# Kernel optimization log

Measured on AMD Instinct MI355X. Metric: run time of the kernel, lower is better.

Reference implementation:

```python
import jax, jax.numpy as jnp
import numpy as np

E, N, D = 800000, 50000, 64

def setup_inputs() -> dict:
    key = jax.random.key(0)
    k0, k1, k2, k3 = jax.random.split(key, 4)
    return {
        "edge_attrs": jax.random.normal(k0, (E, D), dtype=jnp.float32),
        "proj_W": jax.random.normal(k1, (D, D), dtype=jnp.float32) / np.float32(np.sqrt(D)),
        "proj_b": jnp.zeros((D,), dtype=jnp.float32),
        "upd_W": jax.random.normal(k2, (D, D), dtype=jnp.float32) / np.float32(np.sqrt(D)),
        "upd_b": jnp.zeros((D,), dtype=jnp.float32),
        "dst": jax.random.randint(k3, (E,), 0, N, dtype=jnp.int32),
        "n_nodes": N,
    }

def reference(edge_attrs, proj_W, proj_b, upd_W, upd_b, dst, n_nodes):
    # Project each edge attribute: node_projectors[e.type](e.data)
    proj = edge_attrs @ proj_W + proj_b                      # [E, D]
    # Mean-aggregate incoming edges per destination node (MeanAggregator)
    summed = jax.ops.segment_sum(proj, dst, num_segments=n_nodes)          # [N, D]
    counts = jax.ops.segment_sum(jnp.ones((dst.shape[0], 1), proj.dtype),
                                 dst, num_segments=n_nodes)                # [N, 1]
    aggregated = summed / jnp.maximum(counts, 1.0)           # nodes w/o edges -> 0
    # Per-node update: updaters(aggregated)
    return aggregated @ upd_W + upd_b                        # [N, D]
```

## Files before the change

### kernel.cpp

```cpp
#include <hip/hip_runtime.h>
#include <hip/hip_bf16.h>

#define D 64

typedef float f32x4 __attribute__((ext_vector_type(4)));
typedef float f32x2 __attribute__((ext_vector_type(2)));

__global__ void zero_kernel(int4* __restrict__ p, int n4) {
    int i = blockIdx.x * blockDim.x + threadIdx.x;
    if (i < n4) p[i] = make_int4(0, 0, 0, 0);
}

__global__ void count_kernel(const int4* __restrict__ dst4, int* __restrict__ counts, int E4) {
    int i = blockIdx.x * blockDim.x + threadIdx.x;
    if (i < E4) {
        int4 d = dst4[i];
        atomicAdd(&counts[d.x], 1);
        atomicAdd(&counts[d.y], 1);
        atomicAdd(&counts[d.z], 1);
        atomicAdd(&counts[d.w], 1);
    }
}

__global__ void blocksum_kernel(const int* __restrict__ counts, int* __restrict__ bsums, int N) {
    int t = threadIdx.x;
    int i = blockIdx.x * 256 + t;
    int v = (i < N) ? counts[i] : 0;
    int lane = t & 63, wave = t >> 6;
    #pragma unroll
    for (int o = 1; o < 64; o <<= 1) v += __shfl_xor(v, o);
    __shared__ int ws[4];
    if (lane == 0) ws[wave] = v;
    __syncthreads();
    if (t == 0) bsums[blockIdx.x] = ws[0] + ws[1] + ws[2] + ws[3];
}

__global__ void blockscan_kernel(const int* __restrict__ bsums, int* __restrict__ boffs,
                                 int* __restrict__ offsets, int N, int nb,
                                 const float* __restrict__ Wp, const float* __restrict__ Wu,
                                 const float* __restrict__ bp,
                                 float* __restrict__ Wc, float* __restrict__ bc) {
    __shared__ int wsum[16];
    __shared__ float wu[D * D];
    __shared__ float wp[D * D];
    int t = threadIdx.x;
    for (int i = t; i < D * D; i += 1024) { wu[i] = Wu[i]; wp[i] = Wp[i]; }

    int wave = t >> 6, lane = t & 63;
    int v = (t < nb) ? bsums[t] : 0;
    int s = v;
    #pragma unroll
    for (int off = 1; off < 64; off <<= 1) {
        int x = __shfl_up(s, off);
        if (lane >= off) s += x;
    }
    if (lane == 63) wsum[wave] = s;
    __syncthreads();
    int wbase = 0, total = 0;
    #pragma unroll
    for (int w = 0; w < 16; ++w) {
        int x = wsum[w];
        total += x;
        if (w < wave) wbase += x;
    }
    if (t < nb) boffs[t] = s - v + wbase;
    if (t == 0) offsets[N] = total;

    for (int idx = t; idx < D * D; idx += 1024) {
        int d = idx >> 6, j = idx & 63;
        float acc = 0.f;
        #pragma unroll
        for (int k = 0; k < D; ++k) acc = fmaf(wp[d * D + k], wu[k * D + j], acc);
        Wc[idx] = acc;
    }
    if (t < D) {
        float acc = 0.f;
        #pragma unroll
        for (int k = 0; k < D; ++k) acc = fmaf(bp[k], wu[k * D + t], acc);
        bc[t] = acc;
    }
}

__global__ void scatter_scan_kernel(const int* __restrict__ counts, const int* __restrict__ boffs,
                                    int* __restrict__ offsets, int* __restrict__ cursor, int N) {
    int t = threadIdx.x;
    int i = blockIdx.x * 256 + t;
    int v = (i < N) ? counts[i] : 0;
    int lane = t & 63, wave = t >> 6;
    int s = v;
    #pragma unroll
    for (int off = 1; off < 64; off <<= 1) {
        int x = __shfl_up(s, off);
        if (lane >= off) s += x;
    }
    __shared__ int ws[4];
    if (lane == 63) ws[wave] = s;
    __syncthreads();
    int wbase = 0;
    #pragma unroll
    for (int w = 0; w < 4; ++w) if (w < wave) wbase += ws[w];
    int excl = s - v + wbase + boffs[blockIdx.x];
    if (i < N) { offsets[i] = excl; cursor[i] = excl; }
}

__global__ __launch_bounds__(256) void scatter_bf16_kernel(
        const f32x2* __restrict__ attrs2, const int* __restrict__ dst,
        int* __restrict__ cursor, ushort2* __restrict__ ebuf, int E) {
    int lane = threadIdx.x & 63;
    int stride = gridDim.x * 256;
    int E32 = E * 32;
    for (int t = blockIdx.x * 256 + threadIdx.x; t < E32; t += stride) {
        int e = t >> 5, j = t & 31;
        f32x2 v = __builtin_nontemporal_load(&attrs2[t]);
        int pos = 0;
        if ((lane & 31) == 0) pos = atomicAdd(&cursor[dst[e]], 1);
        pos = __shfl(pos, lane & 32);
        unsigned ux = __float_as_uint(v.x);
        unsigned uy = __float_as_uint(v.y);
        ux = (ux + 0x7fffu + ((ux >> 16) & 1u)) >> 16;
        uy = (uy + 0x7fffu + ((uy >> 16) & 1u)) >> 16;
        ebuf[(size_t)pos * 32 + j] = make_ushort2((unsigned short)ux, (unsigned short)uy);
    }
}

__global__ __launch_bounds__(256) void node_kernel(
        const f32x4* __restrict__ ebuf4,
        const int* __restrict__ offsets,
        const float* __restrict__ Wc, const float* __restrict__ bc,
        const float* __restrict__ ub, float* __restrict__ out, int N) {
    __shared__ float wlds[D * D];
    __shared__ float blds[D];
    __shared__ float ulds[D];
    __shared__ int soff[5];
    int t = threadIdx.x;
    int nbase = blockIdx.x * 4;
    if (t < 5) {
        int nn = nbase + t;
        soff[t] = offsets[(nn <= N) ? nn : N];
    }
    #pragma unroll
    for (int i = t; i < D * D; i += 256) wlds[i] = Wc[i];
    if (t < D) { blds[t] = bc[t]; ulds[t] = ub[t]; }
    __syncthreads();

    int wave = t >> 6, lane = t & 63;
    int n = nbase + wave;
    if (n >= N) return;

    int off = soff[wave];
    int off2 = soff[wave + 1];
    int cnt = off2 - off;

    int rsel = lane >> 3;
    int csel = lane & 7;

    float a0 = 0.f, a1 = 0.f, a2 = 0.f, a3 = 0.f, a4 = 0.f, a5 = 0.f, a6 = 0.f, a7 = 0.f;
    for (int r0 = off; r0 < off2; r0 += 8) {
        int row = r0 + rsel;
        bool valid = row < off2;
        int idx = (valid ? row : off) * 8 + csel;
        f32x4 c = ebuf4[idx];
        if (valid) {
            unsigned u0 = __float_as_uint(c.x), u1 = __float_as_uint(c.y);
            unsigned u2 = __float_as_uint(c.z), u3 = __float_as_uint(c.w);
            a0 += __uint_as_float(u0 << 16); a1 += __uint_as_float(u0 & 0xffff0000u);
            a2 += __uint_as_float(u1 << 16); a3 += __uint_as_float(u1 & 0xffff0000u);
            a4 += __uint_as_float(u2 << 16); a5 += __uint_as_float(u2 & 0xffff0000u);
            a6 += __uint_as_float(u3 << 16); a7 += __uint_as_float(u3 & 0xffff0000u);
        }
    }
    #pragma unroll
    for (int mask = 8; mask < 64; mask <<= 1) {
        a0 += __shfl_xor(a0, mask); a1 += __shfl_xor(a1, mask);
        a2 += __shfl_xor(a2, mask); a3 += __shfl_xor(a3, mask);
        a4 += __shfl_xor(a4, mask); a5 += __shfl_xor(a5, mask);
        a6 += __shfl_xor(a6, mask); a7 += __shfl_xor(a7, mask);
    }
    float inv = (cnt > 0) ? 1.f / (float)cnt : 0.f;
    float marr[8] = { a0 * inv, a1 * inv, a2 * inv, a3 * inv,
                      a4 * inv, a5 * inv, a6 * inv, a7 * inv };

    float accO = ulds[lane] + ((cnt > 0) ? blds[lane] : 0.f);
    #pragma unroll
    for (int d = 0; d < D; ++d) {
        float mv = __shfl(marr[d & 7], d >> 3);
        accO = fmaf(mv, wlds[d * D + lane], accO);
    }
    out[(size_t)n * D + lane] = accO;
}

extern "C" void kernel_launch(void* const* d_in, const int* in_sizes, int n_in,
                              void* d_out, int out_size, void* d_ws, size_t ws_size,
                              hipStream_t stream) {
    const float* edge_attrs = (const float*)d_in[0];
    const float* proj_W     = (const float*)d_in[1];
    const float* proj_b     = (const float*)d_in[2];
    const float* upd_W      = (const float*)d_in[3];
    const float* upd_b      = (const float*)d_in[4];
    const int*   dst        = (const int*)d_in[5];

    const int E = in_sizes[0] / D;
    const int N = out_size / D;
    const int nb = (N + 255) / 256;
    const int E4 = E / 4;
    const int N4 = N / 4;

    int*   counts  = (int*)d_ws;
    int*   offsets = counts + N;
    int*   cursor  = offsets + N + 1;
    int*   bsums   = cursor + N;
    int*   boffs   = bsums + nb;
    float* Wc      = (float*)(boffs + nb);
    float* bc      = Wc + D * D;
    size_t ebuf_off = (((size_t)(bc + D) - (size_t)d_ws) + 255) & ~(size_t)255;
    ushort2* ebuf   = (ushort2*)((char*)d_ws + ebuf_off);

    zero_kernel<<<(N4 + 255) / 256, 256, 0, stream>>>((int4*)counts, N4);
    count_kernel<<<(E4 + 255) / 256, 256, 0, stream>>>((const int4*)dst, counts, E4);
    blocksum_kernel<<<nb, 256, 0, stream>>>(counts, bsums, N);
    blockscan_kernel<<<1, 1024, 0, stream>>>(bsums, boffs, offsets, N, nb,
                                             proj_W, upd_W, proj_b, Wc, bc);
    scatter_scan_kernel<<<nb, 256, 0, stream>>>(counts, boffs, offsets, cursor, N);
    scatter_bf16_kernel<<<2048, 256, 0, stream>>>((const f32x2*)edge_attrs, dst,
                                                  cursor, ebuf, E);

    int blocks_n = (N + 3) / 4;
    node_kernel<<<blocks_n, 256, 0, stream>>>((const f32x4*)ebuf, offsets,
                                              Wc, bc, upd_b, (float*)d_out, N);
}
```

Measured before the change: 195.9 us.

## Convert edges in place and gather via CSR index list instead of scattering rows

Edge attributes are now converted to bf16 in their original order, and the per-node counts are taken in the same streaming pass, replacing the scatter of whole rows into node-sorted positions. A separate fill kernel builds a CSR list of edge indices per node, and the node kernel becomes grid-strided and gathers rows through that list. This removes the atomic-serialised scattered 128-byte row writes. In exchange, the node kernel does random row gathers plus an extra index read and an extra kernel launch.

```diff
diff --git a/kernel.cpp b/kernel.cpp
--- a/kernel.cpp
+++ b/kernel.cpp
@@ -11,14 +11,19 @@
     if (i < n4) p[i] = make_int4(0, 0, 0, 0);
 }
 
-__global__ void count_kernel(const int4* __restrict__ dst4, int* __restrict__ counts, int E4) {
-    int i = blockIdx.x * blockDim.x + threadIdx.x;
-    if (i < E4) {
-        int4 d = dst4[i];
-        atomicAdd(&counts[d.x], 1);
-        atomicAdd(&counts[d.y], 1);
-        atomicAdd(&counts[d.z], 1);
-        atomicAdd(&counts[d.w], 1);
+__global__ __launch_bounds__(256) void convert_count_kernel(
+        const f32x2* __restrict__ attrs2, const int* __restrict__ dst,
+        ushort2* __restrict__ ebuf, int* __restrict__ counts, int E32) {
+    int stride = gridDim.x * 256;
+    for (int c = blockIdx.x * 256 + threadIdx.x; c < E32; c += stride) {
+        f32x2 v = __builtin_nontemporal_load(&attrs2[c]);
+        unsigned ux = __float_as_uint(v.x);
+        unsigned uy = __float_as_uint(v.y);
+        ux = (ux + 0x7fffu + ((ux >> 16) & 1u)) >> 16;
+        uy = (uy + 0x7fffu + ((uy >> 16) & 1u)) >> 16;
+        ushort2 pk = make_ushort2((unsigned short)ux, (unsigned short)uy);
+        __builtin_nontemporal_store(*(unsigned*)&pk, (unsigned*)&ebuf[c]);
+        if ((c & 31) == 0) atomicAdd(&counts[dst[c >> 5]], 1);
     }
 }
 
@@ -103,90 +108,81 @@
     if (i < N) { offsets[i] = excl; cursor[i] = excl; }
 }
 
-__global__ __launch_bounds__(256) void scatter_bf16_kernel(
-        const f32x2* __restrict__ attrs2, const int* __restrict__ dst,
-        int* __restrict__ cursor, ushort2* __restrict__ ebuf, int E) {
-    int lane = threadIdx.x & 63;
-    int stride = gridDim.x * 256;
-    int E32 = E * 32;
-    for (int t = blockIdx.x * 256 + threadIdx.x; t < E32; t += stride) {
-        int e = t >> 5, j = t & 31;
-        f32x2 v = __builtin_nontemporal_load(&attrs2[t]);
-        int pos = 0;
-        if ((lane & 31) == 0) pos = atomicAdd(&cursor[dst[e]], 1);
-        pos = __shfl(pos, lane & 32);
-        unsigned ux = __float_as_uint(v.x);
-        unsigned uy = __float_as_uint(v.y);
-        ux = (ux + 0x7fffu + ((ux >> 16) & 1u)) >> 16;
-        uy = (uy + 0x7fffu + ((uy >> 16) & 1u)) >> 16;
-        ebuf[(size_t)pos * 32 + j] = make_ushort2((unsigned short)ux, (unsigned short)uy);
+__global__ void fill_kernel(const int4* __restrict__ dst4, int* __restrict__ cursor,
+                            int* __restrict__ csr, int E4) {
+    int i = blockIdx.x * blockDim.x + threadIdx.x;
+    if (i < E4) {
+        int4 d = dst4[i];
+        int e = i * 4;
+        csr[atomicAdd(&cursor[d.x], 1)] = e + 0;
+        csr[atomicAdd(&cursor[d.y], 1)] = e + 1;
+        csr[atomicAdd(&cursor[d.z], 1)] = e + 2;
+        csr[atomicAdd(&cursor[d.w], 1)] = e + 3;
     }
 }
 
 __global__ __launch_bounds__(256) void node_kernel(
         const f32x4* __restrict__ ebuf4,
-        const int* __restrict__ offsets,
+        const int* __restrict__ csr, const int* __restrict__ offsets,
         const float* __restrict__ Wc, const float* __restrict__ bc,
         const float* __restrict__ ub, float* __restrict__ out, int N) {
     __shared__ float wlds[D * D];
     __shared__ float blds[D];
     __shared__ float ulds[D];
-    __shared__ int soff[5];
-    int t = threadIdx.x;
-    int nbase = blockIdx.x * 4;
-    if (t < 5) {
-        int nn = nbase + t;
-        soff[t] = offsets[(nn <= N) ? nn : N];
-    }
+    int t = threadIdx.x;
     #pragma unroll
     for (int i = t; i < D * D; i += 256) wlds[i] = Wc[i];
     if (t < D) { blds[t] = bc[t]; ulds[t] = ub[t]; }
     __syncthreads();
 
     int wave = t >> 6, lane = t & 63;
-    int n = nbase + wave;
-    if (n >= N) return;
-
-    int off = soff[wave];
-    int off2 = soff[wave + 1];
-    int cnt = off2 - off;
-
     int rsel = lane >> 3;
     int csel = lane & 7;
-
-    float a0 = 0.f, a1 = 0.f, a2 = 0.f, a3 = 0.f, a4 = 0.f, a5 = 0.f, a6 = 0.f, a7 = 0.f;
-    for (int r0 = off; r0 < off2; r0 += 8) {
-        int row = r0 + rsel;
-        bool valid = row < off2;
-        int idx = (valid ? row : off) * 8 + csel;
-        f32x4 c = ebuf4[idx];
-        if (valid) {
-            unsigned u0 = __float_as_uint(c.x), u1 = __float_as_uint(c.y);
-            unsigned u2 = __float_as_uint(c.z), u3 = __float_as_uint(c.w);
-            a0 += __uint_as_float(u0 << 16); a1 += __uint_as_float(u0 & 0xffff0000u);
-            a2 += __uint_as_float(u1 << 16); a3 += __uint_as_float(u1 & 0xffff0000u);
-            a4 += __uint_as_float(u2 << 16); a5 += __uint_as_float(u2 & 0xffff0000u);
-            a6 += __uint_as_float(u3 << 16); a7 += __uint_as_float(u3 & 0xffff0000u);
+    int nwaves = gridDim.x * 4;
+
+    for (int n = blockIdx.x * 4 + wave; n < N; n += nwaves) {
+        int off = offsets[n];
+        int cnt = offsets[n + 1] - off;
+
+        float a0 = 0.f, a1 = 0.f, a2 = 0.f, a3 = 0.f,
+              a4 = 0.f, a5 = 0.f, a6 = 0.f, a7 = 0.f;
+        for (int base = 0; base < cnt; base += 64) {
+            int m = cnt - base; if (m > 64) m = 64;
+            int idxv = (lane < m) ? csr[off + base + lane] : 0;
+            for (int js = 0; js < m; js += 8) {
+                int s = js + rsel;
+                int e = __shfl(idxv, s);
+                bool valid = s < m;
+                f32x4 c = ebuf4[(size_t)(valid ? e : 0) * 8 + csel];
+                if (valid) {
+                    unsigned u0 = __float_as_uint(c.x), u1 = __float_as_uint(c.y);
+                    unsigned u2 = __float_as_uint(c.z), u3 = __float_as_uint(c.w);
+                    a0 += __uint_as_float(u0 << 16); a1 += __uint_as_float(u0 & 0xffff0000u);
+                    a2 += __uint_as_float(u1 << 16); a3 += __uint_as_float(u1 & 0xffff0000u);
+                    a4 += __uint_as_float(u2 << 16); a5 += __uint_as_float(u2 & 0xffff0000u);
+                    a6 += __uint_as_float(u3 << 16); a7 += __uint_as_float(u3 & 0xffff0000u);
+                }
+            }
         }
-    }
-    #pragma unroll
-    for (int mask = 8; mask < 64; mask <<= 1) {
-        a0 += __shfl_xor(a0, mask); a1 += __shfl_xor(a1, mask);
-        a2 += __shfl_xor(a2, mask); a3 += __shfl_xor(a3, mask);
-        a4 += __shfl_xor(a4, mask); a5 += __shfl_xor(a5, mask);
-        a6 += __shfl_xor(a6, mask); a7 += __shfl_xor(a7, mask);
-    }
-    float inv = (cnt > 0) ? 1.f / (float)cnt : 0.f;
-    float marr[8] = { a0 * inv, a1 * inv, a2 * inv, a3 * inv,
-                      a4 * inv, a5 * inv, a6 * inv, a7 * inv };
-
-    float accO = ulds[lane] + ((cnt > 0) ? blds[lane] : 0.f);
-    #pragma unroll
-    for (int d = 0; d < D; ++d) {
-        float mv = __shfl(marr[d & 7], d >> 3);
-        accO = fmaf(mv, wlds[d * D + lane], accO);
-    }
-    out[(size_t)n * D + lane] = accO;
+        #pragma unroll
+        for (int mask = 8; mask < 64; mask <<= 1) {
+            a0 += __shfl_xor(a0, mask); a1 += __shfl_xor(a1, mask);
+            a2 += __shfl_xor(a2, mask); a3 += __shfl_xor(a3, mask);
+            a4 += __shfl_xor(a4, mask); a5 += __shfl_xor(a5, mask);
+            a6 += __shfl_xor(a6, mask); a7 += __shfl_xor(a7, mask);
+        }
+        float inv = (cnt > 0) ? 1.f / (float)cnt : 0.f;
+        float marr[8] = { a0 * inv, a1 * inv, a2 * inv, a3 * inv,
+                          a4 * inv, a5 * inv, a6 * inv, a7 * inv };
+
+        float accO = ulds[lane] + ((cnt > 0) ? blds[lane] : 0.f);
+        #pragma unroll
+        for (int d = 0; d < D; ++d) {
+            float mv = __shfl(marr[d & 7], d >> 3);
+            accO = fmaf(mv, wlds[d * D + lane], accO);
+        }
+        out[(size_t)n * D + lane] = accO;
+    }
 }
 
 extern "C" void kernel_launch(void* const* d_in, const int* in_sizes, int n_in,
@@ -204,27 +200,28 @@
     const int nb = (N + 255) / 256;
     const int E4 = E / 4;
     const int N4 = N / 4;
+    const int E32 = E * 32;
 
     int*   counts  = (int*)d_ws;
     int*   offsets = counts + N;
     int*   cursor  = offsets + N + 1;
     int*   bsums   = cursor + N;
     int*   boffs   = bsums + nb;
-    float* Wc      = (float*)(boffs + nb);
+    int*   csr     = boffs + nb;
+    float* Wc      = (float*)(csr + E);
     float* bc      = Wc + D * D;
     size_t ebuf_off = (((size_t)(bc + D) - (size_t)d_ws) + 255) & ~(size_t)255;
     ushort2* ebuf   = (ushort2*)((char*)d_ws + ebuf_off);
 
     zero_kernel<<<(N4 + 255) / 256, 256, 0, stream>>>((int4*)counts, N4);
-    count_kernel<<<(E4 + 255) / 256, 256, 0, stream>>>((const int4*)dst, counts, E4);
+    convert_count_kernel<<<4096, 256, 0, stream>>>((const f32x2*)edge_attrs, dst,
+                                                   ebuf, counts, E32);
     blocksum_kernel<<<nb, 256, 0, stream>>>(counts, bsums, N);
     blockscan_kernel<<<1, 1024, 0, stream>>>(bsums, boffs, offsets, N, nb,
                                              proj_W, upd_W, proj_b, Wc, bc);
     scatter_scan_kernel<<<nb, 256, 0, stream>>>(counts, boffs, offsets, cursor, N);
-    scatter_bf16_kernel<<<2048, 256, 0, stream>>>((const f32x2*)edge_attrs, dst,
-                                                  cursor, ebuf, E);
-
-    int blocks_n = (N + 3) / 4;
-    node_kernel<<<blocks_n, 256, 0, stream>>>((const f32x4*)ebuf, offsets,
-                                              Wc, bc, upd_b, (float*)d_out, N);
-}
+    fill_kernel<<<(E4 + 255) / 256, 256, 0, stream>>>((const int4*)dst, cursor, csr, E4);
+
+    node_kernel<<<2048, 256, 0, stream>>>((const f32x4*)ebuf, csr, offsets,
+                                          Wc, bc, upd_b, (float*)d_out, N);
+}
```

New measurement: 210.9 us. +7.7%, slower.

## Replace per-node CSR sort with 64-node bins and LDS atomic reduction

Applied to the files above, without the earlier changes.

Edges are now counting-sorted into bins of 64 destination nodes instead of exact per-node CSR order, which removes one scan kernel and reduces cursor atomic contention. Each bin is reduced by one block that accumulates into shared memory with LDS float atomics, then applies the fused projection-update matrix. The change adds a per-edge node-id buffer and LDS atomic traffic. Float summation order becomes nondeterministic. The binscan kernel still runs in a single 1024-thread block, so it relies on nbins (782) being at most 1024.

```diff
diff --git a/kernel.cpp b/kernel.cpp
--- a/kernel.cpp
+++ b/kernel.cpp
@@ -2,9 +2,9 @@
 #include <hip/hip_bf16.h>
 
 #define D 64
+#define BN 64
 
 typedef float f32x4 __attribute__((ext_vector_type(4)));
-typedef float f32x2 __attribute__((ext_vector_type(2)));
 
 __global__ void zero_kernel(int4* __restrict__ p, int n4) {
     int i = blockIdx.x * blockDim.x + threadIdx.x;
@@ -22,24 +22,23 @@
     }
 }
 
-__global__ void blocksum_kernel(const int* __restrict__ counts, int* __restrict__ bsums, int N) {
+__global__ void binsum_kernel(const int* __restrict__ counts, int* __restrict__ bsums,
+                              int N, int nbins) {
     int t = threadIdx.x;
-    int i = blockIdx.x * 256 + t;
-    int v = (i < N) ? counts[i] : 0;
-    int lane = t & 63, wave = t >> 6;
+    int lane = t & 63, w = t >> 6;
+    int bin = blockIdx.x * 4 + w;
+    int i = bin * BN + lane;
+    int v = (bin < nbins && i < N) ? counts[i] : 0;
     #pragma unroll
     for (int o = 1; o < 64; o <<= 1) v += __shfl_xor(v, o);
-    __shared__ int ws[4];
-    if (lane == 0) ws[wave] = v;
-    __syncthreads();
-    if (t == 0) bsums[blockIdx.x] = ws[0] + ws[1] + ws[2] + ws[3];
-}
-
-__global__ void blockscan_kernel(const int* __restrict__ bsums, int* __restrict__ boffs,
-                                 int* __restrict__ offsets, int N, int nb,
-                                 const float* __restrict__ Wp, const float* __restrict__ Wu,
-                                 const float* __restrict__ bp,
-                                 float* __restrict__ Wc, float* __restrict__ bc) {
+    if (lane == 0 && bin < nbins) bsums[bin] = v;
+}
+
+__global__ void binscan_kernel(const int* __restrict__ bsums, int* __restrict__ boffs,
+                               int* __restrict__ bincur, int nbins,
+                               const float* __restrict__ Wp, const float* __restrict__ Wu,
+                               const float* __restrict__ bp,
+                               float* __restrict__ Wc, float* __restrict__ bc) {
     __shared__ int wsum[16];
     __shared__ float wu[D * D];
     __shared__ float wp[D * D];
@@ -47,7 +46,7 @@
     for (int i = t; i < D * D; i += 1024) { wu[i] = Wu[i]; wp[i] = Wp[i]; }
 
     int wave = t >> 6, lane = t & 63;
-    int v = (t < nb) ? bsums[t] : 0;
+    int v = (t < nbins) ? bsums[t] : 0;
     int s = v;
     #pragma unroll
     for (int off = 1; off < 64; off <<= 1) {
@@ -63,8 +62,12 @@
         total += x;
         if (w < wave) wbase += x;
     }
-    if (t < nb) boffs[t] = s - v + wbase;
-    if (t == 0) offsets[N] = total;
+    if (t < nbins) {
+        int excl = s - v + wbase;
+        boffs[t] = excl;
+        bincur[t] = excl;
+    }
+    if (t == 0) boffs[nbins] = total;
 
     for (int idx = t; idx < D * D; idx += 1024) {
         int d = idx >> 6, j = idx & 63;
@@ -81,112 +84,98 @@
     }
 }
 
-__global__ void scatter_scan_kernel(const int* __restrict__ counts, const int* __restrict__ boffs,
-                                    int* __restrict__ offsets, int* __restrict__ cursor, int N) {
-    int t = threadIdx.x;
-    int i = blockIdx.x * 256 + t;
-    int v = (i < N) ? counts[i] : 0;
-    int lane = t & 63, wave = t >> 6;
-    int s = v;
-    #pragma unroll
-    for (int off = 1; off < 64; off <<= 1) {
-        int x = __shfl_up(s, off);
-        if (lane >= off) s += x;
-    }
-    __shared__ int ws[4];
-    if (lane == 63) ws[wave] = s;
-    __syncthreads();
-    int wbase = 0;
-    #pragma unroll
-    for (int w = 0; w < 4; ++w) if (w < wave) wbase += ws[w];
-    int excl = s - v + wbase + boffs[blockIdx.x];
-    if (i < N) { offsets[i] = excl; cursor[i] = excl; }
-}
-
-__global__ __launch_bounds__(256) void scatter_bf16_kernel(
-        const f32x2* __restrict__ attrs2, const int* __restrict__ dst,
-        int* __restrict__ cursor, ushort2* __restrict__ ebuf, int E) {
+__global__ __launch_bounds__(256) void scatter_bin_kernel(
+        const f32x4* __restrict__ attrs4, const int* __restrict__ dst,
+        int* __restrict__ bincur, ushort4* __restrict__ ebin,
+        int* __restrict__ idbin, int E) {
     int lane = threadIdx.x & 63;
-    int stride = gridDim.x * 256;
-    int E32 = E * 32;
-    for (int t = blockIdx.x * 256 + threadIdx.x; t < E32; t += stride) {
-        int e = t >> 5, j = t & 31;
-        f32x2 v = __builtin_nontemporal_load(&attrs2[t]);
-        int pos = 0;
-        if ((lane & 31) == 0) pos = atomicAdd(&cursor[dst[e]], 1);
-        pos = __shfl(pos, lane & 32);
-        unsigned ux = __float_as_uint(v.x);
-        unsigned uy = __float_as_uint(v.y);
-        ux = (ux + 0x7fffu + ((ux >> 16) & 1u)) >> 16;
-        uy = (uy + 0x7fffu + ((uy >> 16) & 1u)) >> 16;
-        ebuf[(size_t)pos * 32 + j] = make_ushort2((unsigned short)ux, (unsigned short)uy);
-    }
-}
-
-__global__ __launch_bounds__(256) void node_kernel(
-        const f32x4* __restrict__ ebuf4,
-        const int* __restrict__ offsets,
-        const float* __restrict__ Wc, const float* __restrict__ bc,
+    int s = lane >> 4;
+    int c = lane & 15;
+    int wid = (blockIdx.x * 256 + threadIdx.x) >> 6;
+    int nw = (gridDim.x * 256) >> 6;
+    for (int e0 = wid * 4; e0 < E; e0 += nw * 4) {
+        int e = e0 + s;
+        f32x4 a = attrs4[(size_t)e * 16 + c];
+        int pos = 0, node = 0;
+        if (c == 0) {
+            node = dst[e];
+            pos = atomicAdd(&bincur[node >> 6], 1);
+        }
+        pos = __shfl(pos, s << 4);
+        unsigned u0 = __float_as_uint(a.x), u1 = __float_as_uint(a.y);
+        unsigned u2 = __float_as_uint(a.z), u3 = __float_as_uint(a.w);
+        u0 = (u0 + 0x7fffu + ((u0 >> 16) & 1u)) >> 16;
+        u1 = (u1 + 0x7fffu + ((u1 >> 16) & 1u)) >> 16;
+        u2 = (u2 + 0x7fffu + ((u2 >> 16) & 1u)) >> 16;
+        u3 = (u3 + 0x7fffu + ((u3 >> 16) & 1u)) >> 16;
+        ushort4 pk = make_ushort4((unsigned short)u0, (unsigned short)u1,
+                                  (unsigned short)u2, (unsigned short)u3);
+        ebin[(size_t)pos * 16 + c] = pk;
+        if (c == 0) idbin[pos] = node;
+    }
+}
+
+__global__ __launch_bounds__(256) void bin_reduce_kernel(
+        const uint4* __restrict__ ebin, const int* __restrict__ idbin,
+        const int* __restrict__ boffs, const int* __restrict__ counts,
+        const float* __restrict__ Wc, const float* __restrict__ bcv,
         const float* __restrict__ ub, float* __restrict__ out, int N) {
+    __shared__ float accum[BN * D];
     __shared__ float wlds[D * D];
     __shared__ float blds[D];
     __shared__ float ulds[D];
-    __shared__ int soff[5];
     int t = threadIdx.x;
-    int nbase = blockIdx.x * 4;
-    if (t < 5) {
-        int nn = nbase + t;
-        soff[t] = offsets[(nn <= N) ? nn : N];
-    }
-    #pragma unroll
+    int b = blockIdx.x;
+    for (int i = t; i < BN * D; i += 256) accum[i] = 0.f;
     for (int i = t; i < D * D; i += 256) wlds[i] = Wc[i];
-    if (t < D) { blds[t] = bc[t]; ulds[t] = ub[t]; }
+    if (t < D) { blds[t] = bcv[t]; ulds[t] = ub[t]; }
     __syncthreads();
 
-    int wave = t >> 6, lane = t & 63;
-    int n = nbase + wave;
-    if (n >= N) return;
-
-    int off = soff[wave];
-    int off2 = soff[wave + 1];
-    int cnt = off2 - off;
-
-    int rsel = lane >> 3;
-    int csel = lane & 7;
-
-    float a0 = 0.f, a1 = 0.f, a2 = 0.f, a3 = 0.f, a4 = 0.f, a5 = 0.f, a6 = 0.f, a7 = 0.f;
-    for (int r0 = off; r0 < off2; r0 += 8) {
-        int row = r0 + rsel;
-        bool valid = row < off2;
-        int idx = (valid ? row : off) * 8 + csel;
-        f32x4 c = ebuf4[idx];
+    int lo = boffs[b], hi = boffs[b + 1];
+    int lane = t & 63, w = t >> 6;
+    int s = lane >> 3;
+    int c = lane & 7;
+    int base0 = b * BN;
+
+    for (int p0 = lo + w * 8; p0 < hi; p0 += 32) {
+        int p = p0 + s;
+        bool valid = p < hi;
+        int node = 0;
+        if (c == 0 && valid) node = idbin[p];
+        node = __shfl(node, lane & 56);
+        uint4 rv = make_uint4(0u, 0u, 0u, 0u);
+        if (valid) rv = ebin[(size_t)p * 8 + c];
         if (valid) {
-            unsigned u0 = __float_as_uint(c.x), u1 = __float_as_uint(c.y);
-            unsigned u2 = __float_as_uint(c.z), u3 = __float_as_uint(c.w);
-            a0 += __uint_as_float(u0 << 16); a1 += __uint_as_float(u0 & 0xffff0000u);
-            a2 += __uint_as_float(u1 << 16); a3 += __uint_as_float(u1 & 0xffff0000u);
-            a4 += __uint_as_float(u2 << 16); a5 += __uint_as_float(u2 & 0xffff0000u);
-            a6 += __uint_as_float(u3 << 16); a7 += __uint_as_float(u3 & 0xffff0000u);
+            int nl = node - base0;
+            float f[8];
+            f[0] = __uint_as_float(rv.x << 16); f[1] = __uint_as_float(rv.x & 0xffff0000u);
+            f[2] = __uint_as_float(rv.y << 16); f[3] = __uint_as_float(rv.y & 0xffff0000u);
+            f[4] = __uint_as_float(rv.z << 16); f[5] = __uint_as_float(rv.z & 0xffff0000u);
+            f[6] = __uint_as_float(rv.w << 16); f[7] = __uint_as_float(rv.w & 0xffff0000u);
+            int abase = nl * D + c * 8;
+            #pragma unroll
+            for (int k = 0; k < 8; ++k) {
+                int kk = (k + s) & 7;
+                atomicAdd(&accum[abase + kk], f[kk]);
+            }
         }
     }
-    #pragma unroll
-    for (int mask = 8; mask < 64; mask <<= 1) {
-        a0 += __shfl_xor(a0, mask); a1 += __shfl_xor(a1, mask);
-        a2 += __shfl_xor(a2, mask); a3 += __shfl_xor(a3, mask);
-        a4 += __shfl_xor(a4, mask); a5 += __shfl_xor(a5, mask);
-        a6 += __shfl_xor(a6, mask); a7 += __shfl_xor(a7, mask);
-    }
-    float inv = (cnt > 0) ? 1.f / (float)cnt : 0.f;
-    float marr[8] = { a0 * inv, a1 * inv, a2 * inv, a3 * inv,
-                      a4 * inv, a5 * inv, a6 * inv, a7 * inv };
-
-    float accO = ulds[lane] + ((cnt > 0) ? blds[lane] : 0.f);
-    #pragma unroll
-    for (int d = 0; d < D; ++d) {
-        float mv = __shfl(marr[d & 7], d >> 3);
-        accO = fmaf(mv, wlds[d * D + lane], accO);
-    }
-    out[(size_t)n * D + lane] = accO;
+    __syncthreads();
+
+    for (int nl = w * 16; nl < w * 16 + 16; ++nl) {
+        int n = base0 + nl;
+        if (n >= N) break;
+        int cnt = counts[n];
+        float inv = (cnt > 0) ? 1.f / (float)cnt : 0.f;
+        float mean = accum[nl * D + lane] * inv;
+        float acc = ulds[lane] + ((cnt > 0) ? blds[lane] : 0.f);
+        #pragma unroll
+        for (int d = 0; d < D; ++d) {
+            float mv = __shfl(mean, d);
+            acc = fmaf(mv, wlds[d * D + lane], acc);
+        }
+        out[(size_t)n * D + lane] = acc;
+    }
 }
 
 extern "C" void kernel_launch(void* const* d_in, const int* in_sizes, int n_in,
@@ -201,30 +190,28 @@
 
     const int E = in_sizes[0] / D;
     const int N = out_size / D;
-    const int nb = (N + 255) / 256;
+    const int nbins = (N + BN - 1) / BN;
     const int E4 = E / 4;
     const int N4 = N / 4;
 
     int*   counts  = (int*)d_ws;
-    int*   offsets = counts + N;
-    int*   cursor  = offsets + N + 1;
-    int*   bsums   = cursor + N;
-    int*   boffs   = bsums + nb;
-    float* Wc      = (float*)(boffs + nb);
+    int*   bsums   = counts + N;
+    int*   boffs   = bsums + nbins;
+    int*   bincur  = boffs + nbins + 1;
+    float* Wc      = (float*)(bincur + nbins);
     float* bc      = Wc + D * D;
-    size_t ebuf_off = (((size_t)(bc + D) - (size_t)d_ws) + 255) & ~(size_t)255;
-    ushort2* ebuf   = (ushort2*)((char*)d_ws + ebuf_off);
+    int*   idbin   = (int*)(bc + D);
+    size_t ebin_off = (((size_t)(idbin + E) - (size_t)d_ws) + 255) & ~(size_t)255;
+    ushort4* ebin   = (ushort4*)((char*)d_ws + ebin_off);
 
     zero_kernel<<<(N4 + 255) / 256, 256, 0, stream>>>((int4*)counts, N4);
     count_kernel<<<(E4 + 255) / 256, 256, 0, stream>>>((const int4*)dst, counts, E4);
-    blocksum_kernel<<<nb, 256, 0, stream>>>(counts, bsums, N);
-    blockscan_kernel<<<1, 1024, 0, stream>>>(bsums, boffs, offsets, N, nb,
-                                             proj_W, upd_W, proj_b, Wc, bc);
-    scatter_scan_kernel<<<nb, 256, 0, stream>>>(counts, boffs, offsets, cursor, N);
-    scatter_bf16_kernel<<<2048, 256, 0, stream>>>((const f32x2*)edge_attrs, dst,
-                                                  cursor, ebuf, E);
-
-    int blocks_n = (N + 3) / 4;
-    node_kernel<<<blocks_n, 256, 0, stream>>>((const f32x4*)ebuf, offsets,
-                                              Wc, bc, upd_b, (float*)d_out, N);
-}
+    binsum_kernel<<<(nbins + 3) / 4, 256, 0, stream>>>(counts, bsums, N, nbins);
+    binscan_kernel<<<1, 1024, 0, stream>>>(bsums, boffs, bincur, nbins,
+                                           proj_W, upd_W, proj_b, Wc, bc);
+    scatter_bin_kernel<<<2048, 256, 0, stream>>>((const f32x4*)edge_attrs, dst,
+                                                 bincur, ebin, idbin, E);
+    bin_reduce_kernel<<<nbins, 256, 0, stream>>>((const uint4*)ebin, idbin, boffs,
+                                                 counts, Wc, bc, upd_b,
+                                                 (float*)d_out, N);
+}
```

Measured after the change: 766.0 us. +291.0%, slower.
